# Kernel tuning notes

Measured on AMD Instinct MI355X. Metric: run time of the kernel, lower is better.

The kernel has to match this reference:

```python
import jax, jax.numpy as jnp
import numpy as np

B, S, D, F, E, K = 4, 4096, 1024, 2048, 8, 2


def setup_inputs() -> dict:
    key = jax.random.key(0)
    ks = jax.random.split(key, 5)
    s = lambda n: 1.0 / np.sqrt(n).astype(np.float32)
    return {
        "hidden_states": jax.random.normal(ks[0], (B, S, D), jnp.float32),
        "router_w": jax.random.normal(ks[1], (E, D), jnp.float32) * s(D),
        "w_gate": jax.random.normal(ks[2], (E, F, D), jnp.float32) * s(D),
        "w_up": jax.random.normal(ks[3], (E, F, D), jnp.float32) * s(D),
        "w_down": jax.random.normal(ks[4], (E, D, F), jnp.float32) * s(F),
    }


def reference(hidden_states, router_w, w_gate, w_up, w_down):
    b, s, d = hidden_states.shape
    e = router_w.shape[0]
    x = hidden_states.reshape(-1, d)  # [T, D], T = B*S

    # --- router: softmax over expert logits, top-k, renormalize (norm_topk_prob) ---
    logits = x @ router_w.T                                   # [T, E]
    scores = jax.nn.softmax(logits.astype(jnp.float32), axis=-1)
    topk_w, topk_idx = jax.lax.top_k(scores, K)               # [T, K]
    topk_w = topk_w / jnp.sum(topk_w, axis=-1, keepdims=True)

    # dense per-(token, expert) combine weight: sum of topk weights routed to e
    cw = jnp.sum(jax.nn.one_hot(topk_idx, e, dtype=topk_w.dtype)
                 * topk_w[..., None], axis=1)                 # [T, E]
    cw = cw.astype(x.dtype)

    # --- experts: SwiGLU MLP per expert, weighted-combined; scan keeps memory low ---
    def per_expert(acc, wts):
        wg, wu, wd, cwe = wts                                  # [F,D],[F,D],[D,F],[T]
        h = jax.nn.silu(x @ wg.T) * (x @ wu.T)                 # [T, F]
        return acc + cwe[:, None] * (h @ wd.T), None

    out, _ = jax.lax.scan(per_expert, jnp.zeros_like(x),
                          (w_gate, w_up, w_down, cw.T))
    return out.reshape(b, s, d)
```

## Files before the change

kernel.cpp:

```cpp
#include <hip/hip_runtime.h>
#include <stdint.h>

#define T_TOK 16384
#define DDIM  1024
#define FDIM  2048
#define NEXP  8
#define MAX_SLOTS 33792
#define NMT (MAX_SLOTS / 128)

typedef __attribute__((ext_vector_type(8))) short bf16x8;
typedef __attribute__((ext_vector_type(4))) float f32x4;

typedef __attribute__((address_space(1))) void gvoid_t;
typedef __attribute__((address_space(3))) void lvoid_t;

#define META_CNT 0
#define META_CUR 256
#define META_OFF 512
#define META_MEXP 544

__device__ __forceinline__ void cp16(void* lds, const void* g) {
  __builtin_amdgcn_global_load_lds((gvoid_t*)g, (lvoid_t*)lds, 16, 0, 0);
}

__device__ __forceinline__ unsigned short f2bf(float f) {
  union { float f; unsigned int u; } v; v.f = f;
  unsigned int u = v.u;
  return (unsigned short)((u + 0x7fffu + ((u >> 16) & 1u)) >> 16);
}

__global__ void router_kernel(const float* __restrict__ x, const float* __restrict__ rw,
                              int* __restrict__ tk_idx, float* __restrict__ tk_w) {
  const int wid = threadIdx.x >> 6;
  const int lane = threadIdx.x & 63;
  const int t = blockIdx.x * 4 + wid;
  const float4* xr = (const float4*)(x + (size_t)t * DDIM);
  float4 xv[4];
#pragma unroll
  for (int i = 0; i < 4; i++) xv[i] = xr[lane + 64 * i];
  float lg[NEXP];
#pragma unroll
  for (int e = 0; e < NEXP; e++) {
    const float4* we = (const float4*)(rw + e * DDIM);
    float s = 0.f;
#pragma unroll
    for (int i = 0; i < 4; i++) {
      float4 v = we[lane + 64 * i];
      s += xv[i].x * v.x + xv[i].y * v.y + xv[i].z * v.z + xv[i].w * v.w;
    }
#pragma unroll
    for (int m = 32; m > 0; m >>= 1) s += __shfl_xor(s, m, 64);
    lg[e] = s;
  }
  int i0 = 0; float m0 = lg[0];
#pragma unroll
  for (int e = 1; e < NEXP; e++) if (lg[e] > m0) { m0 = lg[e]; i0 = e; }
  int i1 = -1; float m1 = -3.0e38f;
#pragma unroll
  for (int e = 0; e < NEXP; e++) if (e != i0 && lg[e] > m1) { m1 = lg[e]; i1 = e; }
  if (lane == 0) {
    float ee = __expf(m1 - m0);
    float w0 = 1.f / (1.f + ee);
    tk_idx[2 * t] = i0; tk_idx[2 * t + 1] = i1;
    tk_w[2 * t] = w0;  tk_w[2 * t + 1] = ee / (1.f + ee);
  }
}

__global__ void hist_kernel(const int* __restrict__ tk_idx, int* __restrict__ meta) {
  int* counts_p = meta + META_CNT;
  int t = blockIdx.x * 256 + threadIdx.x;
  int w = threadIdx.x >> 6, lane = threadIdx.x & 63;
  int e0 = tk_idx[2 * t], e1 = tk_idx[2 * t + 1];
  __shared__ int cnt[4][NEXP];
#pragma unroll
  for (int e = 0; e < NEXP; e++) {
    unsigned long long m0 = __ballot(e0 == e), m1 = __ballot(e1 == e);
    if (lane == 0) cnt[w][e] = __popcll(m0) + __popcll(m1);
  }
  __syncthreads();
  if (threadIdx.x < NEXP) {
    int e = threadIdx.x;
    atomicAdd(&counts_p[e * 32], cnt[0][e] + cnt[1][e] + cnt[2][e] + cnt[3][e]);
  }
}

__global__ void scan_kernel(int* __restrict__ meta) {
  int* counts_p = meta + META_CNT;
  int* offp     = meta + META_OFF;
  int* mexp     = meta + META_MEXP;
  if (threadIdx.x == 0) {
    int acc = 0;
    for (int e = 0; e < NEXP; e++) {
      offp[e] = acc;
      acc += (counts_p[e * 32] + 127) & ~127;
    }
    offp[NEXP] = acc;
    for (int m = 0; m < NMT; m++) {
      int s = m * 128;
      int e = -1;
      for (int q = 0; q < NEXP; q++)
        if (s >= offp[q] && s < offp[q + 1]) { e = q; break; }
      mexp[m] = e;
    }
  }
}

__global__ void scatter_kernel(const int* __restrict__ tk_idx, const float* __restrict__ tk_w,
                               int* __restrict__ meta,
                               int* __restrict__ slot_token, float* __restrict__ slot_w) {
  const int* offp = meta + META_OFF;
  int* cursors_p  = meta + META_CUR;
  int t = blockIdx.x * 256 + threadIdx.x;
  int w = threadIdx.x >> 6, lane = threadIdx.x & 63;
  int e0 = tk_idx[2 * t], e1 = tk_idx[2 * t + 1];
  unsigned long long lmask = (1ull << lane) - 1ull;
  __shared__ int cnt[4][NEXP], woff[4][NEXP], base[NEXP];
  int r0 = 0, r1 = 0;
#pragma unroll
  for (int e = 0; e < NEXP; e++) {
    unsigned long long m0 = __ballot(e0 == e), m1 = __ballot(e1 == e);
    int c0 = __popcll(m0);
    if (lane == 0) cnt[w][e] = c0 + __popcll(m1);
    if (e0 == e) r0 = __popcll(m0 & lmask);
    if (e1 == e) r1 = c0 + __popcll(m1 & lmask);
  }
  __syncthreads();
  if (threadIdx.x < NEXP) {
    int e = threadIdx.x, acc = 0;
#pragma unroll
    for (int ww = 0; ww < 4; ww++) { woff[ww][e] = acc; acc += cnt[ww][e]; }
    base[e] = atomicAdd(&cursors_p[e * 32], acc);
  }
  __syncthreads();
  int p0 = offp[e0] + base[e0] + woff[w][e0] + r0;
  int p1 = offp[e1] + base[e1] + woff[w][e1] + r1;
  slot_token[p0] = t; slot_w[p0] = tk_w[2 * t];
  slot_token[p1] = t; slot_w[p1] = tk_w[2 * t + 1];
}

__global__ void cvt_kernel(const float* __restrict__ src, unsigned short* __restrict__ dst, int n4) {
  int i = blockIdx.x * blockDim.x + threadIdx.x;
  int stride = gridDim.x * blockDim.x;
  for (; i < n4; i += stride) {
    float4 v = ((const float4*)src)[i];
    ushort4 o;
    o.x = f2bf(v.x); o.y = f2bf(v.y); o.z = f2bf(v.z); o.w = f2bf(v.w);
    ((ushort4*)dst)[i] = o;
  }
}

__global__ void gather_kernel(const float* __restrict__ x, const int* __restrict__ slot_token,
                              unsigned short* __restrict__ xg) {
  int slot = blockIdx.x;
  int t = slot_token[slot];
  int c = threadIdx.x * 4;
  ushort4 o;
  if (t >= 0) {
    float4 v = *(const float4*)(x + (size_t)t * DDIM + c);
    o.x = f2bf(v.x); o.y = f2bf(v.y); o.z = f2bf(v.z); o.w = f2bf(v.w);
  } else {
    o.x = 0; o.y = 0; o.z = 0; o.w = 0;
  }
  *(ushort4*)(xg + (size_t)slot * DDIM + c) = o;
}

__global__ __launch_bounds__(256)
void gemm1_kernel(const unsigned short* __restrict__ xg,
                  const unsigned short* __restrict__ wgb,
                  const unsigned short* __restrict__ wub,
                  const int* __restrict__ meta,
                  unsigned short* __restrict__ h, int m0) {
  const int gm = m0 + blockIdx.y;
  const int e = meta[META_MEXP + gm];
  if (e < 0) return;
  const int n0 = blockIdx.x * 64;

  __shared__ alignas(16) unsigned short As[128 * 64];
  __shared__ alignas(16) unsigned short Bgs[64 * 64];
  __shared__ alignas(16) unsigned short Bus[64 * 64];

  const int tid = threadIdx.x;
  const int wid = tid >> 6;
  const int lane = tid & 63;
  const int wr = wid >> 1, wc = wid & 1;

  const unsigned int slog = (unsigned int)(((lane & 7) ^ (lane >> 3)) << 4);
  const char* const xgB = (const char*)xg;
  const char* const wgB = (const char*)wgb + ((size_t)e * FDIM + n0) * (DDIM * 2);
  const char* const wuB = (const char*)wub + ((size_t)e * FDIM + n0) * (DDIM * 2);

  const char* asrc[4]; unsigned int aldc[4];
#pragma unroll
  for (int q = 0; q < 4; q++) {
    int chunk = q * 4 + wid;
    int row = chunk * 8 + (lane >> 3);
    asrc[q] = xgB + (size_t)(gm * 128 + row) * (DDIM * 2) + slog;
    aldc[q] = chunk * 1024;
  }
  const char* bgsrc[2]; const char* busrc[2]; unsigned int bldc[2];
#pragma unroll
  for (int q = 0; q < 2; q++) {
    int chunk = q * 4 + wid;
    int row = chunk * 8 + (lane >> 3);
    bgsrc[q] = wgB + (size_t)row * (DDIM * 2) + slog;
    busrc[q] = wuB + (size_t)row * (DDIM * 2) + slog;
    bldc[q] = chunk * 1024;
  }

  const int lr = lane & 15, lk = lane >> 4;
  const unsigned int fsw = (unsigned int)((lane & 7) << 4);
  unsigned int aoff[4][2], boff[2][2];
#pragma unroll
  for (int mf = 0; mf < 4; mf++)
#pragma unroll
    for (int kc = 0; kc < 2; kc++) {
      unsigned int lg = (unsigned int)(kc * 64 + lk * 16);
      aoff[mf][kc] = (unsigned int)(wr * 64 + mf * 16 + lr) * 128 + (lg ^ fsw);
    }
#pragma unroll
  for (int nf = 0; nf < 2; nf++)
#pragma unroll
    for (int kc = 0; kc < 2; kc++) {
      unsigned int lg = (unsigned int)(kc * 64 + lk * 16);
      boff[nf][kc] = (unsigned int)(wc * 32 + nf * 16 + lr) * 128 + (lg ^ fsw);
    }

  f32x4 accg[4][2] = {};
  f32x4 accu[4][2] = {};
  const char* asb = (const char*)As;
  const char* bgsb = (const char*)Bgs;
  const char* busb = (const char*)Bus;

  for (int kt = 0; kt < DDIM / 64; kt++) {
    const int koff = kt * 128;
#pragma unroll
    for (int q = 0; q < 2; q++) {
      cp16((char*)Bgs + bldc[q], bgsrc[q] + koff);
      cp16((char*)Bus + bldc[q], busrc[q] + koff);
    }
#pragma unroll
    for (int q = 0; q < 4; q++) cp16((char*)As + aldc[q], asrc[q] + koff);
    __syncthreads();
#pragma unroll
    for (int kc = 0; kc < 2; kc++) {
      bf16x8 af[4], bgf[2], buf2[2];
#pragma unroll
      for (int mf = 0; mf < 4; mf++) af[mf] = *(const bf16x8*)(asb + aoff[mf][kc]);
#pragma unroll
      for (int nf = 0; nf < 2; nf++) {
        bgf[nf] = *(const bf16x8*)(bgsb + boff[nf][kc]);
        buf2[nf] = *(const bf16x8*)(busb + boff[nf][kc]);
      }
#pragma unroll
      for (int mf = 0; mf < 4; mf++)
#pragma unroll
        for (int nf = 0; nf < 2; nf++) {
          accg[mf][nf] = __builtin_amdgcn_mfma_f32_16x16x32_bf16(af[mf], bgf[nf], accg[mf][nf], 0, 0, 0);
          accu[mf][nf] = __builtin_amdgcn_mfma_f32_16x16x32_bf16(af[mf], buf2[nf], accu[mf][nf], 0, 0, 0);
        }
    }
    __syncthreads();
  }

  unsigned short* hB = h + (size_t)(gm - m0) * 128 * FDIM;
#pragma unroll
  for (int mf = 0; mf < 4; mf++)
#pragma unroll
    for (int nf = 0; nf < 2; nf++) {
      f32x4 g = accg[mf][nf], u = accu[mf][nf];
#pragma unroll
      for (int j = 0; j < 4; j++) {
        float gv = g[j];
        float hv = (gv / (1.f + __expf(-gv))) * u[j];
        int row = wr * 64 + mf * 16 + lk * 4 + j;
        int col = n0 + wc * 32 + nf * 16 + lr;
        hB[(size_t)row * FDIM + col] = f2bf(hv);
      }
    }
}

__global__ __launch_bounds__(256)
void gemm2_kernel(const unsigned short* __restrict__ h,
                  const unsigned short* __restrict__ wdb,
                  const int* __restrict__ meta,
                  const int* __restrict__ slot_token,
                  const float* __restrict__ slot_w,
                  float* __restrict__ out, int m0) {
  const int gm = m0 + blockIdx.y;
  const int e = meta[META_MEXP + gm];
  if (e < 0) return;
  const int n0 = blockIdx.x * 128;

  __shared__ alignas(16) unsigned short As[128 * 64];
  __shared__ alignas(16) unsigned short Bs[128 * 64];

  const int tid = threadIdx.x;
  const int wid = tid >> 6;
  const int lane = tid & 63;
  const int wr = wid >> 1, wc = wid & 1;

  const unsigned int slog = (unsigned int)(((lane & 7) ^ (lane >> 3)) << 4);
  const char* const hB = (const char*)h + (size_t)(gm - m0) * 128 * (FDIM * 2);
  const char* const wdB = (const char*)wdb + ((size_t)e * DDIM + n0) * (FDIM * 2);

  const char* asrc[4]; const char* bsrc[4]; unsigned int ldc[4];
#pragma unroll
  for (int q = 0; q < 4; q++) {
    int chunk = q * 4 + wid;
    int row = chunk * 8 + (lane >> 3);
    asrc[q] = hB + (size_t)row * (FDIM * 2) + slog;
    bsrc[q] = wdB + (size_t)row * (FDIM * 2) + slog;
    ldc[q] = chunk * 1024;
  }

  const int lr = lane & 15, lk = lane >> 4;
  const unsigned int fsw = (unsigned int)((lane & 7) << 4);
  unsigned int aoff[4][2], boff[4][2];
#pragma unroll
  for (int f = 0; f < 4; f++)
#pragma unroll
    for (int kc = 0; kc < 2; kc++) {
      unsigned int lg = (unsigned int)(kc * 64 + lk * 16);
      aoff[f][kc] = (unsigned int)(wr * 64 + f * 16 + lr) * 128 + (lg ^ fsw);
      boff[f][kc] = (unsigned int)(wc * 64 + f * 16 + lr) * 128 + (lg ^ fsw);
    }

  f32x4 acc[4][4] = {};
  const char* asb = (const char*)As;
  const char* bsb = (const char*)Bs;

  for (int kt = 0; kt < FDIM / 64; kt++) {
    const int koff = kt * 128;
#pragma unroll
    for (int q = 0; q < 4; q++) {
      cp16((char*)As + ldc[q], asrc[q] + koff);
      cp16((char*)Bs + ldc[q], bsrc[q] + koff);
    }
    __syncthreads();
#pragma unroll
    for (int kc = 0; kc < 2; kc++) {
      bf16x8 af[4], bff[4];
#pragma unroll
      for (int mf = 0; mf < 4; mf++) af[mf] = *(const bf16x8*)(asb + aoff[mf][kc]);
#pragma unroll
      for (int nf = 0; nf < 4; nf++) bff[nf] = *(const bf16x8*)(bsb + boff[nf][kc]);
#pragma unroll
      for (int mf = 0; mf < 4; mf++)
#pragma unroll
        for (int nf = 0; nf < 4; nf++)
          acc[mf][nf] = __builtin_amdgcn_mfma_f32_16x16x32_bf16(af[mf], bff[nf], acc[mf][nf], 0, 0, 0);
    }
    __syncthreads();
  }

#pragma unroll
  for (int mf = 0; mf < 4; mf++)
#pragma unroll
    for (int j = 0; j < 4; j++) {
      int slot = gm * 128 + wr * 64 + mf * 16 + lk * 4 + j;
      int tok = slot_token[slot];
      if (tok < 0) continue;
      float w = slot_w[slot];
      float* orow = out + (size_t)tok * DDIM + n0 + wc * 64 + lr;
#pragma unroll
      for (int nf = 0; nf < 4; nf++)
        atomicAdd(orow + nf * 16, w * acc[mf][nf][j]);
    }
}

static constexpr size_t WB       = (size_t)NEXP * FDIM * DDIM * 2;
static constexpr size_t OFF_WG   = 0;
static constexpr size_t OFF_WU   = OFF_WG + WB;
static constexpr size_t OFF_WD   = OFF_WU + WB;
static constexpr size_t OFF_XG   = OFF_WD + WB;
static constexpr size_t XGB      = (size_t)MAX_SLOTS * DDIM * 2;
static constexpr size_t OFF_ST   = OFF_XG + XGB;
static constexpr size_t OFF_SW   = OFF_ST + (size_t)MAX_SLOTS * 4;
static constexpr size_t OFF_TI   = OFF_SW + (size_t)MAX_SLOTS * 4;
static constexpr size_t OFF_TW   = OFF_TI + (size_t)T_TOK * 2 * 4;
static constexpr size_t OFF_META = OFF_TW + (size_t)T_TOK * 2 * 4;
static constexpr size_t OFF_H    = OFF_ST + 1048576;
static constexpr size_t MT_BYTES = (size_t)128 * FDIM * 2;

extern "C" void kernel_launch(void* const* d_in, const int* in_sizes, int n_in,
                              void* d_out, int out_size, void* d_ws, size_t ws_size,
                              hipStream_t stream) {
  const float* x  = (const float*)d_in[0];
  const float* rw = (const float*)d_in[1];
  const float* wg = (const float*)d_in[2];
  const float* wu = (const float*)d_in[3];
  const float* wd = (const float*)d_in[4];
  float* out = (float*)d_out;

  char* ws = (char*)d_ws;
  unsigned short* wgb = (unsigned short*)(ws + OFF_WG);
  unsigned short* wub = (unsigned short*)(ws + OFF_WU);
  unsigned short* wdb = (unsigned short*)(ws + OFF_WD);
  unsigned short* xg  = (unsigned short*)(ws + OFF_XG);
  unsigned short* h   = (unsigned short*)(ws + OFF_H);
  int*   slot_token = (int*)(ws + OFF_ST);
  float* slot_w     = (float*)(ws + OFF_SW);
  int*   tk_idx     = (int*)(ws + OFF_TI);
  float* tk_w       = (float*)(ws + OFF_TW);
  int*   meta       = (int*)(ws + OFF_META);

  size_t avail = ws_size > OFF_H ? ws_size - OFF_H : 0;
  int wmt = (int)(avail / MT_BYTES);
  if (wmt > NMT) wmt = NMT;
  if (wmt < 8) wmt = 8;

  (void)hipMemsetAsync(out, 0, (size_t)out_size * sizeof(float), stream);
  (void)hipMemsetAsync(meta, 0, 2048, stream);
  (void)hipMemsetAsync(slot_token, 0xFF, (size_t)MAX_SLOTS * 4, stream);

  const int W4 = (int)(WB / 2 / 4);
  cvt_kernel<<<4096, 256, 0, stream>>>(wg, wgb, W4);
  cvt_kernel<<<4096, 256, 0, stream>>>(wu, wub, W4);
  cvt_kernel<<<4096, 256, 0, stream>>>(wd, wdb, W4);

  router_kernel<<<T_TOK / 4, 256, 0, stream>>>(x, rw, tk_idx, tk_w);
  hist_kernel<<<T_TOK / 256, 256, 0, stream>>>(tk_idx, meta);
  scan_kernel<<<1, 64, 0, stream>>>(meta);
  scatter_kernel<<<T_TOK / 256, 256, 0, stream>>>(tk_idx, tk_w, meta, slot_token, slot_w);
  gather_kernel<<<MAX_SLOTS, 256, 0, stream>>>(x, slot_token, xg);

  for (int m0 = 0; m0 < NMT; m0 += wmt) {
    int mc = (NMT - m0 < wmt) ? (NMT - m0) : wmt;
    gemm1_kernel<<<dim3(FDIM / 64, mc), 256, 0, stream>>>(xg, wgb, wub, meta, h, m0);
    gemm2_kernel<<<dim3(DDIM / 128, mc), 256, 0, stream>>>(h, wdb, meta, slot_token, slot_w, out, m0);
  }
}
```

Measured before the change: 824.0 us.

## Fuse token gather into gemm1, merge weight conversions, remap blocks across XCDs

The separate gather kernel is removed. The router now writes a bf16 copy of x, and gemm1 reads A rows indirectly through slot_token, so the gathered activation buffer is never materialized. The three weight-conversion launches are merged into one kernel, and the scan kernel's expert-per-tile mapping is parallelized across threads. Both GEMM grids are flattened and remapped so that consecutive blocks sharing an M-tile land on the same XCD for L2 reuse. Padding slots now load token 0's row rather than zeros, which relies on the epilogue skipping tok<0.

```diff
diff --git a/kernel.cpp b/kernel.cpp
--- a/kernel.cpp
+++ b/kernel.cpp
@@ -29,8 +29,16 @@
   return (unsigned short)((u + 0x7fffu + ((u >> 16) & 1u)) >> 16);
 }
 
+__device__ __forceinline__ int xcd_remap(int bid, int nwg) {
+  int xcd = bid & 7, i = bid >> 3;
+  int q = nwg >> 3, r = nwg & 7;
+  int base = (xcd < r) ? xcd * (q + 1) : r * (q + 1) + (xcd - r) * q;
+  return base + i;
+}
+
 __global__ void router_kernel(const float* __restrict__ x, const float* __restrict__ rw,
-                              int* __restrict__ tk_idx, float* __restrict__ tk_w) {
+                              int* __restrict__ tk_idx, float* __restrict__ tk_w,
+                              unsigned short* __restrict__ xb) {
   const int wid = threadIdx.x >> 6;
   const int lane = threadIdx.x & 63;
   const int t = blockIdx.x * 4 + wid;
@@ -38,6 +46,13 @@
   float4 xv[4];
 #pragma unroll
   for (int i = 0; i < 4; i++) xv[i] = xr[lane + 64 * i];
+  ushort4* xbr = (ushort4*)(xb + (size_t)t * DDIM);
+#pragma unroll
+  for (int i = 0; i < 4; i++) {
+    ushort4 o;
+    o.x = f2bf(xv[i].x); o.y = f2bf(xv[i].y); o.z = f2bf(xv[i].z); o.w = f2bf(xv[i].w);
+    xbr[lane + 64 * i] = o;
+  }
   float lg[NEXP];
 #pragma unroll
   for (int e = 0; e < NEXP; e++) {
@@ -88,20 +103,23 @@
   int* counts_p = meta + META_CNT;
   int* offp     = meta + META_OFF;
   int* mexp     = meta + META_MEXP;
+  __shared__ int soff[NEXP + 1];
   if (threadIdx.x == 0) {
     int acc = 0;
     for (int e = 0; e < NEXP; e++) {
-      offp[e] = acc;
+      offp[e] = acc; soff[e] = acc;
       acc += (counts_p[e * 32] + 127) & ~127;
     }
-    offp[NEXP] = acc;
-    for (int m = 0; m < NMT; m++) {
-      int s = m * 128;
-      int e = -1;
-      for (int q = 0; q < NEXP; q++)
-        if (s >= offp[q] && s < offp[q + 1]) { e = q; break; }
-      mexp[m] = e;
-    }
+    offp[NEXP] = acc; soff[NEXP] = acc;
+  }
+  __syncthreads();
+  for (int m = threadIdx.x; m < NMT; m += blockDim.x) {
+    int s = m * 128;
+    int e = -1;
+#pragma unroll
+    for (int q = 0; q < NEXP; q++)
+      if (s >= soff[q] && s < soff[q + 1]) { e = q; break; }
+    mexp[m] = e;
   }
 }
 
@@ -138,42 +156,36 @@
   slot_token[p1] = t; slot_w[p1] = tk_w[2 * t + 1];
 }
 
-__global__ void cvt_kernel(const float* __restrict__ src, unsigned short* __restrict__ dst, int n4) {
+#define W4EACH (1 << 22)
+__global__ void cvt3_kernel(const float* __restrict__ wg, const float* __restrict__ wu,
+                            const float* __restrict__ wd,
+                            unsigned short* __restrict__ wgb, unsigned short* __restrict__ wub,
+                            unsigned short* __restrict__ wdb) {
   int i = blockIdx.x * blockDim.x + threadIdx.x;
   int stride = gridDim.x * blockDim.x;
-  for (; i < n4; i += stride) {
-    float4 v = ((const float4*)src)[i];
+  for (; i < 3 * W4EACH; i += stride) {
+    int which = i >> 22, j = i & (W4EACH - 1);
+    const float4* s = (const float4*)(which == 0 ? wg : which == 1 ? wu : wd);
+    ushort4* d = (ushort4*)(which == 0 ? wgb : which == 1 ? wub : wdb);
+    float4 v = s[j];
     ushort4 o;
     o.x = f2bf(v.x); o.y = f2bf(v.y); o.z = f2bf(v.z); o.w = f2bf(v.w);
-    ((ushort4*)dst)[i] = o;
-  }
-}
-
-__global__ void gather_kernel(const float* __restrict__ x, const int* __restrict__ slot_token,
-                              unsigned short* __restrict__ xg) {
-  int slot = blockIdx.x;
-  int t = slot_token[slot];
-  int c = threadIdx.x * 4;
-  ushort4 o;
-  if (t >= 0) {
-    float4 v = *(const float4*)(x + (size_t)t * DDIM + c);
-    o.x = f2bf(v.x); o.y = f2bf(v.y); o.z = f2bf(v.z); o.w = f2bf(v.w);
-  } else {
-    o.x = 0; o.y = 0; o.z = 0; o.w = 0;
-  }
-  *(ushort4*)(xg + (size_t)slot * DDIM + c) = o;
+    d[j] = o;
+  }
 }
 
 __global__ __launch_bounds__(256)
-void gemm1_kernel(const unsigned short* __restrict__ xg,
+void gemm1_kernel(const unsigned short* __restrict__ xb,
                   const unsigned short* __restrict__ wgb,
                   const unsigned short* __restrict__ wub,
                   const int* __restrict__ meta,
+                  const int* __restrict__ slot_token,
                   unsigned short* __restrict__ h, int m0) {
-  const int gm = m0 + blockIdx.y;
+  const int wgid = xcd_remap((int)blockIdx.x, (int)gridDim.x);
+  const int gm = m0 + (wgid >> 5);
   const int e = meta[META_MEXP + gm];
   if (e < 0) return;
-  const int n0 = blockIdx.x * 64;
+  const int n0 = (wgid & 31) * 64;
 
   __shared__ alignas(16) unsigned short As[128 * 64];
   __shared__ alignas(16) unsigned short Bgs[64 * 64];
@@ -185,7 +197,7 @@
   const int wr = wid >> 1, wc = wid & 1;
 
   const unsigned int slog = (unsigned int)(((lane & 7) ^ (lane >> 3)) << 4);
-  const char* const xgB = (const char*)xg;
+  const char* const xbB = (const char*)xb;
   const char* const wgB = (const char*)wgb + ((size_t)e * FDIM + n0) * (DDIM * 2);
   const char* const wuB = (const char*)wub + ((size_t)e * FDIM + n0) * (DDIM * 2);
 
@@ -194,7 +206,9 @@
   for (int q = 0; q < 4; q++) {
     int chunk = q * 4 + wid;
     int row = chunk * 8 + (lane >> 3);
-    asrc[q] = xgB + (size_t)(gm * 128 + row) * (DDIM * 2) + slog;
+    int tok = slot_token[gm * 128 + row];
+    tok = tok < 0 ? 0 : tok;
+    asrc[q] = xbB + (size_t)tok * (DDIM * 2) + slog;
     aldc[q] = chunk * 1024;
   }
   const char* bgsrc[2]; const char* busrc[2]; unsigned int bldc[2];
@@ -286,10 +300,11 @@
                   const int* __restrict__ slot_token,
                   const float* __restrict__ slot_w,
                   float* __restrict__ out, int m0) {
-  const int gm = m0 + blockIdx.y;
+  const int wgid = xcd_remap((int)blockIdx.x, (int)gridDim.x);
+  const int gm = m0 + (wgid >> 3);
   const int e = meta[META_MEXP + gm];
   if (e < 0) return;
-  const int n0 = blockIdx.x * 128;
+  const int n0 = (wgid & 7) * 128;
 
   __shared__ alignas(16) unsigned short As[128 * 64];
   __shared__ alignas(16) unsigned short Bs[128 * 64];
@@ -372,9 +387,9 @@
 static constexpr size_t OFF_WG   = 0;
 static constexpr size_t OFF_WU   = OFF_WG + WB;
 static constexpr size_t OFF_WD   = OFF_WU + WB;
-static constexpr size_t OFF_XG   = OFF_WD + WB;
-static constexpr size_t XGB      = (size_t)MAX_SLOTS * DDIM * 2;
-static constexpr size_t OFF_ST   = OFF_XG + XGB;
+static constexpr size_t OFF_XB   = OFF_WD + WB;
+static constexpr size_t XBB      = (size_t)T_TOK * DDIM * 2;
+static constexpr size_t OFF_ST   = OFF_XB + XBB;
 static constexpr size_t OFF_SW   = OFF_ST + (size_t)MAX_SLOTS * 4;
 static constexpr size_t OFF_TI   = OFF_SW + (size_t)MAX_SLOTS * 4;
 static constexpr size_t OFF_TW   = OFF_TI + (size_t)T_TOK * 2 * 4;
@@ -396,7 +411,7 @@
   unsigned short* wgb = (unsigned short*)(ws + OFF_WG);
   unsigned short* wub = (unsigned short*)(ws + OFF_WU);
   unsigned short* wdb = (unsigned short*)(ws + OFF_WD);
-  unsigned short* xg  = (unsigned short*)(ws + OFF_XG);
+  unsigned short* xb  = (unsigned short*)(ws + OFF_XB);
   unsigned short* h   = (unsigned short*)(ws + OFF_H);
   int*   slot_token = (int*)(ws + OFF_ST);
   float* slot_w     = (float*)(ws + OFF_SW);
@@ -413,20 +428,15 @@
   (void)hipMemsetAsync(meta, 0, 2048, stream);
   (void)hipMemsetAsync(slot_token, 0xFF, (size_t)MAX_SLOTS * 4, stream);
 
-  const int W4 = (int)(WB / 2 / 4);
-  cvt_kernel<<<4096, 256, 0, stream>>>(wg, wgb, W4);
-  cvt_kernel<<<4096, 256, 0, stream>>>(wu, wub, W4);
-  cvt_kernel<<<4096, 256, 0, stream>>>(wd, wdb, W4);
-
-  router_kernel<<<T_TOK / 4, 256, 0, stream>>>(x, rw, tk_idx, tk_w);
+  cvt3_kernel<<<4096, 256, 0, stream>>>(wg, wu, wd, wgb, wub, wdb);
+  router_kernel<<<T_TOK / 4, 256, 0, stream>>>(x, rw, tk_idx, tk_w, xb);
   hist_kernel<<<T_TOK / 256, 256, 0, stream>>>(tk_idx, meta);
-  scan_kernel<<<1, 64, 0, stream>>>(meta);
+  scan_kernel<<<1, 256, 0, stream>>>(meta);
   scatter_kernel<<<T_TOK / 256, 256, 0, stream>>>(tk_idx, tk_w, meta, slot_token, slot_w);
-  gather_kernel<<<MAX_SLOTS, 256, 0, stream>>>(x, slot_token, xg);
 
   for (int m0 = 0; m0 < NMT; m0 += wmt) {
     int mc = (NMT - m0 < wmt) ? (NMT - m0) : wmt;
-    gemm1_kernel<<<dim3(FDIM / 64, mc), 256, 0, stream>>>(xg, wgb, wub, meta, h, m0);
-    gemm2_kernel<<<dim3(DDIM / 128, mc), 256, 0, stream>>>(h, wdb, meta, slot_token, slot_w, out, m0);
-  }
-}
+    gemm1_kernel<<<mc * 32, 256, 0, stream>>>(xb, wgb, wub, meta, slot_token, h, m0);
+    gemm2_kernel<<<mc * 8, 256, 0, stream>>>(h, wdb, meta, slot_token, slot_w, out, m0);
+  }
+}
```

Result: faster. 759.1 us (-7.9%).
